# Performance work log

Measured on AMD Instinct MI355X. Metric: run time of the kernel, lower is better.

The kernel has to match this reference:

```python
import jax, jax.numpy as jnp
import numpy as np

B, S, D, H, DFF, STEPS = 8, 1024, 512, 8, 2048, 6
EPS = 1e-6
HALT_EPS = 0.01
PONDER_BIAS_INIT = 1.0


def setup_inputs() -> dict:
    key = jax.random.key(0)
    ks = jax.random.split(key, 24)
    w = lambda k, shape, s=0.02: jax.random.normal(k, shape, dtype=jnp.float32) * s
    inp = {
        "x": jax.random.normal(ks[0], (B, S, D), dtype=jnp.float32),
        # multi-head attention projections (shared across ACT steps)
        "wq": w(ks[1], (D, D)), "bq": jnp.zeros((D,), jnp.float32),
        "wk": w(ks[2], (D, D)), "bk": jnp.zeros((D,), jnp.float32),
        "wv": w(ks[3], (D, D)), "bv": jnp.zeros((D,), jnp.float32),
        "wo": w(ks[4], (D, D)), "bo": jnp.zeros((D,), jnp.float32),
        # point-wise FFN: Dense(dff, relu) -> LayerNorm -> Dense(d_model)
        "w1": w(ks[5], (D, DFF)), "b1": jnp.zeros((DFF,), jnp.float32),
        "lnf_g": jnp.ones((DFF,), jnp.float32), "lnf_b": jnp.zeros((DFF,), jnp.float32),
        "w2": w(ks[6], (DFF, D)), "b2": jnp.zeros((D,), jnp.float32),
        # post-attention / post-FFN layernorms
        "ln1_g": jnp.ones((D,), jnp.float32), "ln1_b": jnp.zeros((D,), jnp.float32),
        "ln2_g": jnp.ones((D,), jnp.float32), "ln2_b": jnp.zeros((D,), jnp.float32),
        # ACT ponder kernel: Dense(1, sigmoid) with ponder_bias_init
        "act_w": w(ks[7], (D, 1)),
        "act_b": jnp.full((1,), PONDER_BIAS_INIT, jnp.float32),
    }
    return inp


def layer_norm(x, g, b):
    m = jnp.mean(x, axis=-1, keepdims=True)
    v = jnp.var(x, axis=-1, keepdims=True)
    return (x - m) * jax.lax.rsqrt(v + EPS) * g + b


def reference(x, wq, bq, wk, bk, wv, bv, wo, bo, w1, b1, lnf_g, lnf_b, w2, b2,
              ln1_g, ln1_b, ln2_g, ln2_b, act_w, act_b):
    dh = D // H
    scale = 1.0 / jnp.sqrt(jnp.float32(dh))

    def split_heads(t):  # [B,S,D] -> [B,H,S,dh]
        return t.reshape(B, S, H, dh).transpose(0, 2, 1, 3)

    def enc_layer(st):
        q = split_heads(st @ wq + bq)
        k = split_heads(st @ wk + bk)
        v = split_heads(st @ wv + bv)
        logits = jnp.einsum('bhqd,bhkd->bhqk', q, k) * scale
        attn = jax.nn.softmax(logits, axis=-1)
        ctx = jnp.einsum('bhqk,bhkd->bhqd', attn, v)
        ctx = ctx.transpose(0, 2, 1, 3).reshape(B, S, D)
        out1 = layer_norm(st + (ctx @ wo + bo), ln1_g, ln1_b)
        h = layer_norm(jax.nn.relu(out1 @ w1 + b1), lnf_g, lnf_b)
        return layer_norm(out1 + (h @ w2 + b2), ln2_g, ln2_b)

    thr = 1.0 - HALT_EPS

    def step(carry, _):
        st, hp, rem, nup = carry
        p = jax.nn.sigmoid(st @ act_w + act_b)[..., 0]  # [B,S]
        still = (hp < 1.0).astype(jnp.float32)
        cand = hp + p * still
        new_halted = (cand > thr).astype(jnp.float32) * still
        still = (cand <= thr).astype(jnp.float32) * still
        hp = hp + p * still
        rem = rem + new_halted * (1.0 - hp)
        hp = hp + new_halted * rem
        nup = nup + still + new_halted
        uw = (p * still + new_halted * rem)[..., None]  # [B,S,1]
        new_st = enc_layer(st)
        st = new_st * uw + st * (1.0 - uw)
        return (st, hp, rem, nup), None

    z = jnp.zeros((B, S), jnp.float32)
    (st, hp, rem, nup), _ = jax.lax.scan(step, (x, z, z, z), None, length=STEPS)
    return st
```

## Files before the change

### kernel.cpp

```cpp
#include <hip/hip_runtime.h>
#include <cstdint>
#include <cstddef>

#define B_ 8
#define S_ 1024
#define D_ 512
#define H_ 8
#define DFF_ 2048
#define STEPS_ 6
#define M_ (B_*S_)

typedef unsigned short u16;
typedef u16   u16x8 __attribute__((ext_vector_type(8)));
typedef short s16x8 __attribute__((ext_vector_type(8)));
typedef float f32x4 __attribute__((ext_vector_type(4)));
typedef float f32x16 __attribute__((ext_vector_type(16)));

__device__ __forceinline__ u16 f2b(float f){
  union { float f; unsigned u; } v; v.f = f;
  unsigned r = v.u + 0x7fffu + ((v.u >> 16) & 1u);
  return (u16)(r >> 16);
}
__device__ __forceinline__ float b2f(u16 u){
  union { unsigned u; float f; } v; v.u = ((unsigned)u) << 16;
  return v.f;
}
__device__ __forceinline__ unsigned cvtpk(float lo, float hi){
  unsigned r;
  asm("v_cvt_pk_bf16_f32 %0, %1, %2" : "=v"(r) : "v"(lo), "v"(hi));
  return r;
}
__device__ __forceinline__ void gload16(const void* g, void* l){
  __builtin_amdgcn_global_load_lds(
    (const __attribute__((address_space(1))) void*)g,
    (__attribute__((address_space(3))) void*)l, 16, 0, 0);
}
__device__ __forceinline__ float wred_sum(float v){
  #pragma unroll
  for (int m = 1; m < 64; m <<= 1) v += __shfl_xor(v, m, 64);
  return v;
}

__global__ __launch_bounds__(256) void prep_kernel(const float* __restrict__ x,
    const float* __restrict__ aw, const float* __restrict__ ab,
    float* __restrict__ st, u16* __restrict__ stb,
    float* __restrict__ hp, float* __restrict__ rem, float* __restrict__ uw){
  int tid = threadIdx.x; int l = tid & 63; int w = tid >> 6;
  size_t i = (size_t)blockIdx.x*256 + tid;
  const float4* xp = (const float4*)x + i*2;
  float4 a = xp[0], b = xp[1];
  ((float4*)st)[i*2]   = a;
  ((float4*)st)[i*2+1] = b;
  u16x8 o;
  o[0]=f2b(a.x); o[1]=f2b(a.y); o[2]=f2b(a.z); o[3]=f2b(a.w);
  o[4]=f2b(b.x); o[5]=f2b(b.y); o[6]=f2b(b.z); o[7]=f2b(b.w);
  ((u16x8*)stb)[i] = o;
  const float4* wp = (const float4*)aw + (size_t)l*2;
  float4 w0 = wp[0], w1 = wp[1];
  float d = a.x*w0.x + a.y*w0.y + a.z*w0.z + a.w*w0.w
          + b.x*w1.x + b.y*w1.y + b.z*w1.z + b.w*w1.w;
  d = wred_sum(d);
  if (l == 0){
    int row = blockIdx.x*4 + w;
    float t = d + ab[0];
    float p = 1.f / (1.f + expf(-t));
    float nh  = (p > 0.99f) ? 1.f : 0.f;
    float st2 = 1.f - nh;
    float h = p*st2;
    float r = nh*(1.f - h);
    h += nh*r;
    hp[row] = h; rem[row] = r;
    uw[row] = p*st2 + nh*r;
  }
}

__global__ __launch_bounds__(256) void tcast_kernel(const float* __restrict__ W,
    u16* __restrict__ Wt, int K, int N, const float* __restrict__ scale){
  __shared__ u16 T[64*66];
  int tid = threadIdx.x;
  int nbt = N >> 6;
  int k0 = (blockIdx.x / nbt) << 6, n0 = (blockIdx.x % nbt) << 6;
  int r = tid >> 2, c4 = tid & 3;
  float sc = scale ? scale[k0 + r] : 1.f;
  const float* src = W + (size_t)(k0 + r)*N + n0 + c4*16;
  #pragma unroll
  for (int q = 0; q < 2; q++){
    float4 f0 = ((const float4*)src)[q*2], f1 = ((const float4*)src)[q*2+1];
    u16x8 t;
    t[0]=f2b(f0.x*sc); t[1]=f2b(f0.y*sc); t[2]=f2b(f0.z*sc); t[3]=f2b(f0.w*sc);
    t[4]=f2b(f1.x*sc); t[5]=f2b(f1.y*sc); t[6]=f2b(f1.z*sc); t[7]=f2b(f1.w*sc);
    *(u16x8*)&T[r*66 + c4*16 + q*8] = t;
  }
  __syncthreads();
  int n = tid >> 2;
  #pragma unroll
  for (int t2 = 0; t2 < 2; t2++){
    int sc2 = (tid & 3) + t2*4;
    u16x8 o;
    #pragma unroll
    for (int j = 0; j < 8; j++) o[j] = T[(sc2*8 + j)*66 + n];
    *(u16x8*)&Wt[(size_t)(n0 + n)*K + k0 + sc2*8] = o;
  }
}

__global__ void packb_kernel(const float* __restrict__ bq, const float* __restrict__ bk,
                             const float* __restrict__ bv, float* __restrict__ bqkv,
                             unsigned* __restrict__ flags){
  int i = blockIdx.x*256 + threadIdx.x;
  if (i < 512)       bqkv[i] = bq[i];
  else if (i < 1024) bqkv[i] = bk[i-512];
  else if (i < 1536) bqkv[i] = bv[i-1024];
  if (blockIdx.x == 0 && threadIdx.x < 256){
    int t = threadIdx.x;
    flags[t] = (t < 64 || (t >= 128 && t < 192)) ? 1u : 0u;
  }
}

__global__ __launch_bounds__(256) void gcpart_kernel(const float* __restrict__ W,
    const float* __restrict__ g, const float* __restrict__ be,
    float* __restrict__ pg, float* __restrict__ pc, int N){
  int kb = blockIdx.x, cb = blockIdx.y, t = threadIdx.x;
  __shared__ float gs[64], bs[64];
  if (t < 64){ gs[t] = g[kb*64 + t]; bs[t] = be[kb*64 + t]; }
  __syncthreads();
  int col = cb*256 + t;
  float ag = 0.f, ac = 0.f;
  #pragma unroll 8
  for (int k = 0; k < 64; k++){
    float w = W[(size_t)(kb*64 + k)*N + col];
    ag = fmaf(gs[k], w, ag);
    ac = fmaf(bs[k], w, ac);
  }
  pg[(size_t)kb*N + col] = ag;
  pc[(size_t)kb*N + col] = ac;
}

__global__ __launch_bounds__(256) void gcred_kernel(const float* __restrict__ pg,
    const float* __restrict__ pc, float* __restrict__ G, float* __restrict__ Cc,
    int np, int N){
  int col = blockIdx.x*256 + threadIdx.x;
  float sg = 0.f, sc = 0.f;
  for (int i = 0; i < np; i++){
    sg += pg[(size_t)i*N + col];
    sc += pc[(size_t)i*N + col];
  }
  G[col] = sg; Cc[col] = sc;
}

__global__ __launch_bounds__(256) void stats_kernel(const float2* __restrict__ parts,
    float2* __restrict__ stats, int np, float invD,
    const unsigned* __restrict__ tfact, unsigned* __restrict__ zeroA,
    unsigned* __restrict__ zeroB){
  if (zeroA && blockIdx.x == 0){
    int t = threadIdx.x;
    if (t < 64) zeroA[t] = 0u;
    else if (t < 128) zeroB[t-64] = 0u;
  }
  int tok = blockIdx.x*256 + threadIdx.x;
  if (!tfact[tok >> 7]) return;
  float s = 0.f, q = 0.f;
  for (int i = 0; i < np; i++){
    float2 p = parts[(size_t)i*M_ + tok];
    s += p.x; q += p.y;
  }
  float mu = s*invD;
  float var = q*invD - mu*mu;
  stats[tok] = make_float2(mu, rsqrtf(fmaxf(var, 0.f) + 1e-6f));
}

template<int EPI>
__global__ __launch_bounds__(256) void gemm128_kernel(
    const u16* __restrict__ A, const u16* __restrict__ Bt,
    const float* __restrict__ bias, void* __restrict__ C,
    int ntn, int K, int ldo, u16* __restrict__ vt,
    const float2* __restrict__ strow, const float* __restrict__ gvec,
    const float* __restrict__ cvec, float2* __restrict__ parts,
    const float* __restrict__ resid, const unsigned* __restrict__ tflag,
    const unsigned* __restrict__ actarr){
  __shared__ u16 Als[2][128*64];
  __shared__ u16 Bls[2][128*64];
  int tid = threadIdx.x, l = tid & 63, w = tid >> 6;
  int hi = l >> 4, ln = l & 15;
  int wm = w >> 1, wn = w & 1;
  int nwg = gridDim.x;
  int bid = blockIdx.x;
  int swz = (bid & 7) * (nwg >> 3) + (bid >> 3);
  int tn = swz % ntn, tm = swz / ntn;
  if (actarr){
    unsigned any = 0;
    #pragma unroll
    for (int i = 0; i < 64; i += 8)
      any |= actarr[i] | actarr[i+1] | actarr[i+2] | actarr[i+3]
           | actarr[i+4] | actarr[i+5] | actarr[i+6] | actarr[i+7];
    if (!any) return;
  }
  if (!tflag[tm]) return;
  int m0 = tm << 7, n0 = tn << 7;
  int rl8 = l >> 3;
  int cg = (l & 7) ^ rl8;
  size_t aoff = (size_t)(m0 + w*8 + rl8)*K + cg*8;
  size_t boff = (size_t)(n0 + w*8 + rl8)*K + cg*8;
  int nt = K >> 6;

  f32x4 acc[4][4];
  #pragma unroll
  for (int i=0;i<4;i++)
    #pragma unroll
    for (int j=0;j<4;j++) acc[i][j] = (f32x4){0.f,0.f,0.f,0.f};

  #define G128(buf, kt) do { \
    size_t kof = (size_t)(kt)*64; \
    _Pragma("unroll") \
    for (int j = 0; j < 4; j++){ \
      gload16(A  + aoff + (size_t)j*32*K + kof, &Als[buf][(j*4 + w)*512]); \
      gload16(Bt + boff + (size_t)j*32*K + kof, &Bls[buf][(j*4 + w)*512]); \
    } } while(0)

  G128(0, 0);
  asm volatile("s_waitcnt vmcnt(0)" ::: "memory");
  __builtin_amdgcn_s_barrier();
  __builtin_amdgcn_sched_barrier(0);

  for (int t = 0; t < nt; t++){
    int cur = t & 1;
    if (t+1 < nt) G128(cur^1, t+1);
    s16x8 af[4][2], bf[4][2];
    #pragma unroll
    for (int mi=0;mi<4;mi++){
      int row = wm*64 + mi*16 + ln;
      #pragma unroll
      for (int kk=0;kk<2;kk++)
        af[mi][kk] = *(const s16x8*)&Als[cur][row*64 + (((kk*4+hi)^(row&7))*8)];
    }
    #pragma unroll
    for (int ni=0;ni<4;ni++){
      int row = wn*64 + ni*16 + ln;
      #pragma unroll
      for (int kk=0;kk<2;kk++)
        bf[ni][kk] = *(const s16x8*)&Bls[cur][row*64 + (((kk*4+hi)^(row&7))*8)];
    }
    asm volatile("s_waitcnt lgkmcnt(0)" ::: "memory");
    __builtin_amdgcn_sched_barrier(0);
    __builtin_amdgcn_s_setprio(1);
    #pragma unroll
    for (int mi=0;mi<4;mi++)
      #pragma unroll
      for (int ni=0;ni<4;ni++)
        #pragma unroll
        for (int kk=0;kk<2;kk++)
          acc[mi][ni] = __builtin_amdgcn_mfma_f32_16x16x32_bf16(af[mi][kk], bf[ni][kk], acc[mi][ni], 0,0,0);
    __builtin_amdgcn_s_setprio(0);
    if (t+1 < nt){
      asm volatile("s_waitcnt vmcnt(0)" ::: "memory");
      __builtin_amdgcn_s_barrier();
      __builtin_amdgcn_sched_barrier(0);
    }
  }
  #undef G128

  if (EPI == 1){
    if (n0 >= 1024){
      #pragma unroll
      for (int mi=0;mi<4;mi++){
        int row0 = m0 + wm*64 + mi*16 + hi*4;
        int b = row0 >> 10, s0 = row0 & 1023;
        #pragma unroll
        for (int ni=0;ni<4;ni++){
          int vcol = (n0 - 1024) + wn*64 + ni*16 + ln;
          int h = vcol >> 6, d = vcol & 63;
          float bc = bias[1024 + vcol];
          uint2 pk;
          pk.x = cvtpk(acc[mi][ni][0] + bc, acc[mi][ni][1] + bc);
          pk.y = cvtpk(acc[mi][ni][2] + bc, acc[mi][ni][3] + bc);
          *(uint2*)&vt[((size_t)((b*8 + h)*64 + d))*1024 + s0] = pk;
        }
      }
      return;
    }
    float qs = (n0 < 512) ? 0.125f : 1.0f;
    #pragma unroll
    for (int mi=0;mi<4;mi++){
      int row0 = m0 + wm*64 + mi*16 + hi*4;
      #pragma unroll
      for (int ni=0;ni<4;ni++){
        int col = n0 + wn*64 + ni*16 + ln;
        float bc = bias[col];
        #pragma unroll
        for (int r=0;r<4;r++)
          ((u16*)C)[(size_t)(row0+r)*ldo + col] = f2b((acc[mi][ni][r] + bc)*qs);
      }
    }
    return;
  }

  if (EPI == 3){
    float bv[4];
    #pragma unroll
    for (int ni=0;ni<4;ni++) bv[ni] = bias[n0 + wn*64 + ni*16 + ln];
    #pragma unroll
    for (int mi=0;mi<4;mi++){
      int row0 = m0 + wm*64 + mi*16 + hi*4;
      #pragma unroll
      for (int r=0;r<4;r++){
        int row = row0 + r;
        float s = 0.f, q = 0.f;
        #pragma unroll
        for (int ni=0;ni<4;ni++){
          int col = n0 + wn*64 + ni*16 + ln;
          float v = acc[mi][ni][r] + bv[ni] + resid[(size_t)row*ldo + col];
          ((u16*)C)[(size_t)row*ldo + col] = f2b(v);
          s += v; q += v*v;
        }
        #pragma unroll
        for (int msk=1;msk<16;msk<<=1){ s += __shfl_xor(s,msk,64); q += __shfl_xor(q,msk,64); }
        if (ln == 0) parts[(size_t)(tn*2 + wn)*M_ + row] = make_float2(s, q);
      }
    }
    return;
  }

  {
    float gv[4], cv[4];
    #pragma unroll
    for (int ni=0;ni<4;ni++){
      int col = n0 + wn*64 + ni*16 + ln;
      gv[ni] = gvec[col];
      cv[ni] = cvec[col] + bias[col];
    }
    #pragma unroll
    for (int mi=0;mi<4;mi++){
      int row0 = m0 + wm*64 + mi*16 + hi*4;
      #pragma unroll
      for (int r=0;r<4;r++){
        int row = row0 + r;
        float2 sr = strow[row];
        float rmu = sr.y * sr.x;
        float s = 0.f, q = 0.f;
        #pragma unroll
        for (int ni=0;ni<4;ni++){
          int col = n0 + wn*64 + ni*16 + ln;
          float v = sr.y*acc[mi][ni][r] - rmu*gv[ni] + cv[ni];
          if (EPI == 4) v = fmaxf(v, 0.f);
          ((u16*)C)[(size_t)row*ldo + col] = f2b(v);
          s += v; q += v*v;
        }
        if (EPI == 4){
          #pragma unroll
          for (int msk=1;msk<16;msk<<=1){ s += __shfl_xor(s,msk,64); q += __shfl_xor(q,msk,64); }
          if (ln == 0) parts[(size_t)(tn*2 + wn)*M_ + row] = make_float2(s, q);
        }
      }
    }
  }
}

__global__ __launch_bounds__(256) void attn_kernel(const u16* __restrict__ qkv,
                                                   const u16* __restrict__ vt,
                                                   u16* __restrict__ ctx,
                                                   const unsigned* __restrict__ tfact){
  __shared__ u16 Ks[2][64*64];
  __shared__ u16 Vs[2][64*64];
  int tid = threadIdx.x, l = tid & 63, w = tid >> 6;
  int q5 = l & 31, hi2 = l >> 5;
  int orig = ((blockIdx.x & 7) << 6) | (blockIdx.x >> 3);
  int qt = orig & 7, h = (orig >> 3) & 7, b = orig >> 6;
  if (!tfact[b*8 + qt]) return;
  size_t rowbase = (size_t)b * S_;

  int qrow = qt*128 + w*32 + q5;
  s16x8 bq[4];
  #pragma unroll
  for (int dk = 0; dk < 4; dk++)
    bq[dk] = *(const s16x8*)&qkv[(rowbase + qrow)*1536 + h*64 + dk*16 + hi2*8];

  int rl = l >> 3;
  int cg = (l & 7) ^ rl;
  const u16* kb = qkv + rowbase*1536 + 512 + h*64 + cg*8;
  const u16* vb = vt + (size_t)((b*8 + h)*64)*1024 + cg*8;

  f32x16 o[2];
  #pragma unroll
  for (int mt = 0; mt < 2; mt++)
    #pragma unroll
    for (int r = 0; r < 16; r++) o[mt][r] = 0.f;
  float l_ = 0.f;

  #define STAGE(buf, kt) do { \
    _Pragma("unroll") \
    for (int r2 = 0; r2 < 2; r2++){ \
      int rr = r2*32 + w*8; \
      gload16(kb + (size_t)((kt)*64 + rr + rl)*1536, &Ks[buf][rr*64]); \
      gload16(vb + (size_t)(rr + rl)*1024 + (kt)*64, &Vs[buf][rr*64]); \
    } } while(0)

  STAGE(0, 0);
  STAGE(1, 1);
  asm volatile("s_waitcnt vmcnt(4)" ::: "memory");
  __builtin_amdgcn_s_barrier();
  __builtin_amdgcn_sched_barrier(0);

  for (int kt = 0; kt < 16; kt++){
    int cur = kt & 1;
    s16x8 ak[2][4], av[2][4];
    #pragma unroll
    for (int mt = 0; mt < 2; mt++){
      int r0 = mt*32 + q5;
      int sw = r0 & 7;
      #pragma unroll
      for (int dk = 0; dk < 4; dk++)
        ak[mt][dk] = *(const s16x8*)&Ks[cur][r0*64 + (((2*dk + hi2) ^ sw)*8)];
      #pragma unroll
      for (int ks = 0; ks < 4; ks++)
        av[mt][ks] = *(const s16x8*)&Vs[cur][r0*64 + (((2*ks + hi2) ^ sw)*8)];
    }
    asm volatile("s_waitcnt lgkmcnt(0)" ::: "memory");
    __builtin_amdgcn_sched_barrier(0);
    __builtin_amdgcn_s_barrier();
    __builtin_amdgcn_sched_barrier(0);
    if (kt < 14) STAGE(cur, kt+2);

    f32x16 sacc[2];
    #pragma unroll
    for (int mt = 0; mt < 2; mt++){
      f32x16 acc;
      #pragma unroll
      for (int r = 0; r < 16; r++) acc[r] = 0.f;
      #pragma unroll
      for (int dk = 0; dk < 4; dk++)
        acc = __builtin_amdgcn_mfma_f32_32x32x16_bf16(ak[mt][dk], bq[dk], acc, 0,0,0);
      sacc[mt] = acc;
    }

    float p[2][16];
    float rs = 0.f;
    #pragma unroll
    for (int mt = 0; mt < 2; mt++)
      #pragma unroll
      for (int r = 0; r < 16; r++){
        float e = __expf(sacc[mt][r]);
        p[mt][r] = e; rs += e;
      }
    rs += __shfl_xor(rs, 32, 64);
    l_ += rs;

    unsigned wds[4][4];
    #pragma unroll
    for (int ks = 0; ks < 4; ks++){
      const int mt = ks >> 1, base = (ks & 1)*8;
      unsigned a0 = cvtpk(p[mt][base+0], p[mt][base+1]);
      unsigned b0 = cvtpk(p[mt][base+4], p[mt][base+5]);
      asm("v_permlane32_swap_b32 %0, %1" : "+v"(a0), "+v"(b0));
      unsigned a1 = cvtpk(p[mt][base+2], p[mt][base+3]);
      unsigned b1 = cvtpk(p[mt][base+6], p[mt][base+7]);
      asm("v_permlane32_swap_b32 %0, %1" : "+v"(a1), "+v"(b1));
      wds[ks][0] = a0; wds[ks][1] = a1; wds[ks][2] = b0; wds[ks][3] = b1;
    }

    #pragma unroll
    for (int ks = 0; ks < 4; ks++){
      union { unsigned u[4]; s16x8 v; } bp;
      bp.u[0] = wds[ks][0]; bp.u[1] = wds[ks][1];
      bp.u[2] = wds[ks][2]; bp.u[3] = wds[ks][3];
      #pragma unroll
      for (int mt = 0; mt < 2; mt++)
        o[mt] = __builtin_amdgcn_mfma_f32_32x32x16_bf16(av[mt][ks], bp.v, o[mt], 0,0,0);
    }

    if (kt < 15){
      if (kt < 14) asm volatile("s_waitcnt vmcnt(4)" ::: "memory");
      else         asm volatile("s_waitcnt vmcnt(0)" ::: "memory");
      __builtin_amdgcn_s_barrier();
      __builtin_amdgcn_sched_barrier(0);
    }
  }
  #undef STAGE

  __builtin_amdgcn_s_barrier();
  float inv = 1.f / l_;
  u16* ob = ((w < 2) ? (u16*)Ks : (u16*)Vs) + (w & 1)*2304;
  #pragma unroll
  for (int mt = 0; mt < 2; mt++)
    #pragma unroll
    for (int g = 0; g < 4; g++)
      #pragma unroll
      for (int p2 = 0; p2 < 2; p2++){
        unsigned wd = cvtpk(o[mt][g*4 + p2*2]*inv, o[mt][g*4 + p2*2 + 1]*inv);
        int d0 = mt*32 + g*8 + hi2*4 + p2*2;
        *(unsigned*)&ob[q5*72 + d0] = wd;
      }
  asm volatile("s_waitcnt lgkmcnt(0)" ::: "memory");
  __builtin_amdgcn_sched_barrier(0);
  int r2 = l >> 1, cb = (l & 1)*32;
  size_t row = rowbase + qt*128 + w*32 + r2;
  #pragma unroll
  for (int c = 0; c < 4; c++){
    uint4 v = *(uint4*)&ob[r2*72 + cb + c*8];
    *(uint4*)&ctx[row*512 + h*64 + cb + c*8] = v;
  }
}

__global__ __launch_bounds__(256) void ln2mix_kernel(
    const u16* __restrict__ yb, const u16* __restrict__ o2b,
    const float2* __restrict__ st1,
    const float* __restrict__ g1, const float* __restrict__ be1,
    const float* __restrict__ g, const float* __restrict__ bt,
    const float* __restrict__ aw, const float* __restrict__ ab,
    float* __restrict__ st, u16* __restrict__ stb,
    float* __restrict__ hp, float* __restrict__ rem, float* __restrict__ uw,
    unsigned* __restrict__ tfact_next, unsigned* __restrict__ tfchg_next){
  int lane = threadIdx.x & 63;
  int row = blockIdx.x*4 + (threadIdx.x >> 6);
  float u = uw[row];
  if (u == 0.f) return;
  size_t base = (size_t)row*512 + lane*8;
  float2 s1 = st1[row];
  float mu1 = s1.x, rstd1 = s1.y;
  int c0 = lane*8;
  float v[8], sv[8];
  {
    u16x8 y8 = *(const u16x8*)(yb + base);
    u16x8 o8 = *(const u16x8*)(o2b + base);
    const float4* sp = (const float4*)(st + base);
    float4 s0 = sp[0], s1f = sp[1];
    #pragma unroll
    for (int j=0;j<8;j++){
      float out1 = (b2f(y8[j]) - mu1)*rstd1*g1[c0+j] + be1[c0+j];
      v[j] = out1 + b2f(o8[j]);
    }
    sv[0]=s0.x; sv[1]=s0.y; sv[2]=s0.z; sv[3]=s0.w;
    sv[4]=s1f.x; sv[5]=s1f.y; sv[6]=s1f.z; sv[7]=s1f.w;
  }
  float sum=0.f, sq=0.f;
  #pragma unroll
  for (int j=0;j<8;j++){ sum += v[j]; sq += v[j]*v[j]; }
  sum = wred_sum(sum); sq = wred_sum(sq);
  float mean = sum*(1.f/512.f);
  float var  = sq*(1.f/512.f) - mean*mean;
  float rstd = rsqrtf(fmaxf(var, 0.f) + 1e-6f);
  float um1 = 1.f - u;
  float z[8]; u16x8 ob;
  #pragma unroll
  for (int j=0;j<8;j++){
    float y = (v[j]-mean)*rstd*g[c0+j] + bt[c0+j];
    z[j] = y*u + sv[j]*um1;
    ob[j] = f2b(z[j]);
  }
  float4* op = (float4*)(st + base);
  op[0] = make_float4(z[0],z[1],z[2],z[3]);
  op[1] = make_float4(z[4],z[5],z[6],z[7]);
  *(u16x8*)(stb + base) = ob;
  const float4* wp = (const float4*)aw + (size_t)lane*2;
  float4 w0 = wp[0], w1 = wp[1];
  float d = z[0]*w0.x + z[1]*w0.y + z[2]*w0.z + z[3]*w0.w
          + z[4]*w1.x + z[5]*w1.y + z[6]*w1.z + z[7]*w1.w;
  d = wred_sum(d);
  if (lane == 0){
    float t = d + ab[0];
    float p = 1.f / (1.f + expf(-t));
    float h = hp[row], r = rem[row];
    bool active_next = (h < 1.f);
    float still = active_next ? 1.f : 0.f;
    float cand  = h + p*still;
    float nh  = (cand > 0.99f)  ? still : 0.f;
    float st2 = (cand <= 0.99f) ? still : 0.f;
    h += p*st2;
    r += nh*(1.f - h);
    h += nh*r;
    hp[row] = h; rem[row] = r;
    uw[row] = p*st2 + nh*r;
    tfchg_next[row >> 7] = 1u;
    if (active_next) tfact_next[row >> 7] = 1u;
  }
}

extern "C" void kernel_launch(void* const* d_in, const int* in_sizes, int n_in,
                              void* d_out, int out_size, void* d_ws, size_t ws_size,
                              hipStream_t stream){
  const float* x     = (const float*)d_in[0];
  const float* wq    = (const float*)d_in[1];
  const float* bq    = (const float*)d_in[2];
  const float* wk    = (const float*)d_in[3];
  const float* bk    = (const float*)d_in[4];
  const float* wv    = (const float*)d_in[5];
  const float* bv    = (const float*)d_in[6];
  const float* wo    = (const float*)d_in[7];
  const float* bo    = (const float*)d_in[8];
  const float* w1    = (const float*)d_in[9];
  const float* b1    = (const float*)d_in[10];
  const float* lnf_g = (const float*)d_in[11];
  const float* lnf_b = (const float*)d_in[12];
  const float* w2    = (const float*)d_in[13];
  const float* b2    = (const float*)d_in[14];
  const float* ln1_g = (const float*)d_in[15];
  const float* ln1_b = (const float*)d_in[16];
  const float* ln2_g = (const float*)d_in[17];
  const float* ln2_b = (const float*)d_in[18];
  const float* aw    = (const float*)d_in[19];
  const float* ab    = (const float*)d_in[20];
  float* st = (float*)d_out;

  char* cur = (char*)d_ws;
  auto alloc = [&](size_t n){ void* p = cur; cur += (n + 255) & ~(size_t)255; return p; };
  u16*  wqkv_t = (u16*)alloc((size_t)1536*512*2);
  u16*  wo_t   = (u16*)alloc((size_t)512*512*2);
  u16*  w1_t   = (u16*)alloc((size_t)2048*512*2);
  u16*  w2_t   = (u16*)alloc((size_t)512*2048*2);
  float* bqkv  = (float*)alloc(1536*4);
  float* G1    = (float*)alloc(2048*4);
  float* C1    = (float*)alloc(2048*4);
  float* G2    = (float*)alloc(512*4);
  float* C2    = (float*)alloc(512*4);
  float* pg    = (float*)alloc((size_t)16384*4);
  float* pc    = (float*)alloc((size_t)16384*4);
  u16*  stb    = (u16*)alloc((size_t)M_*512*2);
  u16*  qkv    = (u16*)alloc((size_t)M_*1536*2);
  u16*  vt     = (u16*)alloc((size_t)M_*512*2);
  u16*  ctx    = (u16*)alloc((size_t)M_*512*2);
  u16*  yb     = (u16*)alloc((size_t)M_*512*2);
  u16*  o2b    = (u16*)alloc((size_t)M_*512*2);
  u16*  hbuf   = (u16*)alloc((size_t)M_*2048*2);
  float2* parts1 = (float2*)alloc((size_t)16*M_*8);
  float2* parts2 = (float2*)alloc((size_t)32*M_*8);
  float2* stats1 = (float2*)alloc((size_t)M_*8);
  float2* stats2 = (float2*)alloc((size_t)M_*8);
  float* halt  = (float*)alloc((size_t)3*M_*4);
  unsigned* flags = (unsigned*)alloc(256*4);
  float* hp = halt, *rem = halt + M_, *uw = halt + 2*M_;

  prep_kernel<<<2048, 256, 0, stream>>>(x, aw, ab, st, stb, hp, rem, uw);
  packb_kernel<<<6, 256, 0, stream>>>(bq, bk, bv, bqkv, flags);
  tcast_kernel<<<64,  256, 0, stream>>>(wq, wqkv_t,            512, 512, nullptr);
  tcast_kernel<<<64,  256, 0, stream>>>(wk, wqkv_t + 512*512,  512, 512, nullptr);
  tcast_kernel<<<64,  256, 0, stream>>>(wv, wqkv_t + 1024*512, 512, 512, nullptr);
  tcast_kernel<<<64,  256, 0, stream>>>(wo, wo_t, 512, 512, nullptr);
  tcast_kernel<<<256, 256, 0, stream>>>(w1, w1_t, 512, 2048, ln1_g);
  tcast_kernel<<<256, 256, 0, stream>>>(w2, w2_t, 2048, 512, lnf_g);
  gcpart_kernel<<<dim3(8, 8),  256, 0, stream>>>(w1, ln1_g, ln1_b, pg, pc, 2048);
  gcred_kernel<<<8, 256, 0, stream>>>(pg, pc, G1, C1, 8, 2048);
  gcpart_kernel<<<dim3(32, 2), 256, 0, stream>>>(w2, lnf_g, lnf_b, pg, pc, 512);
  gcred_kernel<<<2, 256, 0, stream>>>(pg, pc, G2, C2, 32, 512);

  for (int s = 0; s < STEPS_; s++){
    unsigned* act_c = flags + (s & 1)*64;
    unsigned* act_n = flags + ((s+1) & 1)*64;
    unsigned* chg_c = flags + 128 + (s & 1)*64;
    unsigned* chg_n = flags + 128 + ((s+1) & 1)*64;
    gemm128_kernel<1><<<64*12, 256, 0, stream>>>(stb, wqkv_t, bqkv, qkv, 12, 512, 1536,
                                                 vt, nullptr, nullptr, nullptr, nullptr, nullptr,
                                                 chg_c, act_c);
    attn_kernel<<<512, 256, 0, stream>>>(qkv, vt, ctx, act_c);
    gemm128_kernel<3><<<64*4, 256, 0, stream>>>(ctx, wo_t, bo, yb, 4, 512, 512,
                                                nullptr, nullptr, nullptr, nullptr, parts1, st,
                                                act_c, nullptr);
    stats_kernel<<<M_/256, 256, 0, stream>>>(parts1, stats1, 8, 1.f/512.f,
                                             act_c, nullptr, nullptr);
    gemm128_kernel<4><<<64*16, 256, 0, stream>>>(yb, w1_t, b1, hbuf, 16, 512, 2048,
                                                 nullptr, stats1, G1, C1, parts2, nullptr,
                                                 act_c, nullptr);
    stats_kernel<<<M_/256, 256, 0, stream>>>(parts2, stats2, 32, 1.f/2048.f,
                                             act_c, act_n, chg_n);
    gemm128_kernel<5><<<64*4, 256, 0, stream>>>(hbuf, w2_t, b2, o2b, 4, 2048, 512,
                                                nullptr, stats2, G2, C2, nullptr, nullptr,
                                                act_c, nullptr);
    ln2mix_kernel<<<M_/4, 256, 0, stream>>>(yb, o2b, stats1, ln1_g, ln1_b, ln2_g, ln2_b,
                                            aw, ab, st, stb, hp, rem, uw, act_n, chg_n);
  }
}
```

Before: 594.9 us.

## Use triple-buffered K=32 LDS pipeline in 128x128 GEMM

Changes the GEMM main loop from a double-buffered K=64 tile to a triple-buffered K=32 tile. Global loads run two stages ahead, and the wait is relaxed to vmcnt(4) so that one stage's loads stay in flight during compute. LDS use drops from 64KB to 48KB, and the XOR swizzle is adapted to 32-wide rows. The trade-off is twice as many barriers and iterations, each with fewer MFMAs, in exchange for deeper prefetch and possibly higher occupancy.

```diff
diff --git a/kernel.cpp b/kernel.cpp
--- a/kernel.cpp
+++ b/kernel.cpp
@@ -177,8 +177,8 @@
     const float* __restrict__ cvec, float2* __restrict__ parts,
     const float* __restrict__ resid, const unsigned* __restrict__ tflag,
     const unsigned* __restrict__ actarr){
-  __shared__ u16 Als[2][128*64];
-  __shared__ u16 Bls[2][128*64];
+  __shared__ u16 Als[3][128*32];
+  __shared__ u16 Bls[3][128*32];
   int tid = threadIdx.x, l = tid & 63, w = tid >> 6;
   int hi = l >> 4, ln = l & 15;
   int wm = w >> 1, wn = w & 1;
@@ -196,11 +196,11 @@
   }
   if (!tflag[tm]) return;
   int m0 = tm << 7, n0 = tn << 7;
-  int rl8 = l >> 3;
-  int cg = (l & 7) ^ rl8;
-  size_t aoff = (size_t)(m0 + w*8 + rl8)*K + cg*8;
-  size_t boff = (size_t)(n0 + w*8 + rl8)*K + cg*8;
-  int nt = K >> 6;
+  int rl4 = l >> 2, cl4 = l & 3;
+  int cg = cl4 ^ ((rl4 >> 1) & 3);
+  size_t aoff = (size_t)(m0 + rl4)*K + cg*8;
+  size_t boff = (size_t)(n0 + rl4)*K + cg*8;
+  int nt = K >> 5;
 
   f32x4 acc[4][4];
   #pragma unroll
@@ -209,35 +209,32 @@
     for (int j=0;j<4;j++) acc[i][j] = (f32x4){0.f,0.f,0.f,0.f};
 
   #define G128(buf, kt) do { \
-    size_t kof = (size_t)(kt)*64; \
+    size_t kof = (size_t)(kt)*32; \
     _Pragma("unroll") \
-    for (int j = 0; j < 4; j++){ \
-      gload16(A  + aoff + (size_t)j*32*K + kof, &Als[buf][(j*4 + w)*512]); \
-      gload16(Bt + boff + (size_t)j*32*K + kof, &Bls[buf][(j*4 + w)*512]); \
+    for (int j = 0; j < 2; j++){ \
+      gload16(A  + aoff + (size_t)(j*4 + w)*16*K + kof, &Als[buf][(j*4 + w)*512]); \
+      gload16(Bt + boff + (size_t)(j*4 + w)*16*K + kof, &Bls[buf][(j*4 + w)*512]); \
     } } while(0)
 
   G128(0, 0);
-  asm volatile("s_waitcnt vmcnt(0)" ::: "memory");
+  G128(1, 1);
+  asm volatile("s_waitcnt vmcnt(4)" ::: "memory");
   __builtin_amdgcn_s_barrier();
   __builtin_amdgcn_sched_barrier(0);
 
   for (int t = 0; t < nt; t++){
-    int cur = t & 1;
-    if (t+1 < nt) G128(cur^1, t+1);
-    s16x8 af[4][2], bf[4][2];
+    int rb = t % 3;
+    if (t+2 < nt){ int pb = (t+2) % 3; G128(pb, t+2); }
+    s16x8 af[4], bf[4];
     #pragma unroll
     for (int mi=0;mi<4;mi++){
       int row = wm*64 + mi*16 + ln;
-      #pragma unroll
-      for (int kk=0;kk<2;kk++)
-        af[mi][kk] = *(const s16x8*)&Als[cur][row*64 + (((kk*4+hi)^(row&7))*8)];
+      af[mi] = *(const s16x8*)&Als[rb][row*32 + ((hi ^ ((row>>1)&3))*8)];
     }
     #pragma unroll
     for (int ni=0;ni<4;ni++){
       int row = wn*64 + ni*16 + ln;
-      #pragma unroll
-      for (int kk=0;kk<2;kk++)
-        bf[ni][kk] = *(const s16x8*)&Bls[cur][row*64 + (((kk*4+hi)^(row&7))*8)];
+      bf[ni] = *(const s16x8*)&Bls[rb][row*32 + ((hi ^ ((row>>1)&3))*8)];
     }
     asm volatile("s_waitcnt lgkmcnt(0)" ::: "memory");
     __builtin_amdgcn_sched_barrier(0);
@@ -246,12 +243,11 @@
     for (int mi=0;mi<4;mi++)
       #pragma unroll
       for (int ni=0;ni<4;ni++)
-        #pragma unroll
-        for (int kk=0;kk<2;kk++)
-          acc[mi][ni] = __builtin_amdgcn_mfma_f32_16x16x32_bf16(af[mi][kk], bf[ni][kk], acc[mi][ni], 0,0,0);
+        acc[mi][ni] = __builtin_amdgcn_mfma_f32_16x16x32_bf16(af[mi], bf[ni], acc[mi][ni], 0,0,0);
     __builtin_amdgcn_s_setprio(0);
     if (t+1 < nt){
-      asm volatile("s_waitcnt vmcnt(0)" ::: "memory");
+      if (t+2 < nt) asm volatile("s_waitcnt vmcnt(4)" ::: "memory");
+      else          asm volatile("s_waitcnt vmcnt(0)" ::: "memory");
       __builtin_amdgcn_s_barrier();
       __builtin_amdgcn_sched_barrier(0);
     }
```

After: 644.4 us. +8.3%, slower.
